# Optimization experiments

Measured on AMD Instinct MI355X. Metric: run time of the kernel, lower is better.

Reference implementation:

```python
import jax, jax.numpy as jnp
import numpy as np

EMBED_DIM = 2048
HIDDEN_DIM = 2048
SEQ_LEN = 8192


def setup_inputs() -> dict:
    key = jax.random.key(0)
    ks = jax.random.split(key, 6)
    x = jax.random.normal(ks[0], (SEQ_LEN, EMBED_DIM), dtype=jnp.float32)
    # original uses torch.rand (uniform [0,1)) for params
    W_h = jax.random.uniform(ks[1], (HIDDEN_DIM, HIDDEN_DIM), dtype=jnp.float32)
    W_x = jax.random.uniform(ks[2], (HIDDEN_DIM, EMBED_DIM), dtype=jnp.float32)
    W_y = jax.random.uniform(ks[3], (EMBED_DIM, HIDDEN_DIM), dtype=jnp.float32)
    B_h = jax.random.uniform(ks[4], (HIDDEN_DIM,), dtype=jnp.float32)
    B_y = jax.random.uniform(ks[5], (EMBED_DIM,), dtype=jnp.float32)
    return {"x": x, "W_h": W_h, "W_x": W_x, "W_y": W_y, "B_h": B_h, "B_y": B_y}


def reference(x, W_h, W_x, W_y, B_h, B_y):
    # Precompute input projections for all timesteps in one GEMM: [T, H]
    xp = x @ W_x.T + B_h

    def step(h, xp_t):
        h_new = jnp.tanh(W_h @ h + xp_t)  # [H]
        return h_new, h_new

    h0 = jnp.zeros((W_h.shape[0],), dtype=x.dtype)
    h_final, hs = jax.lax.scan(step, h0, xp)  # hs: [T, H]
    # Output projection + softmax over embed dim, batched over timesteps
    logits = hs @ W_y.T + B_y  # [T, E]
    output = jax.nn.softmax(logits, axis=-1)
    return (h_final, output)
```

## Files before the change

### kernel.cpp

```cpp
#include <hip/hip_runtime.h>

#define T_SEQ 8192
#define HDIM  2048
#define EDIM  2048
#define RBLK  64
#define ROWS_PER_BLK (HDIM / RBLK)

typedef unsigned long long u64;
typedef __attribute__((ext_vector_type(4))) unsigned int u32x4;
typedef __attribute__((ext_vector_type(4))) float f32x4;

__device__ inline void poll_pair(const u64* p0, const u64* p1, u32x4& a, u32x4& b) {
    asm volatile("global_load_dwordx4 %0, %2, off sc1\n\t"
                 "global_load_dwordx4 %1, %3, off sc1\n\t"
                 "s_waitcnt vmcnt(0)"
                 : "=v"(a), "=v"(b) : "v"(p0), "v"(p1) : "memory");
}

__device__ inline f32x4 ld_w16(const float* p) {
    f32x4 r;
    asm volatile("global_load_dwordx4 %0, %1, off" : "=v"(r) : "v"(p));
    return r;
}

__global__ __launch_bounds__(256) void gemm_nt_bias(
    const float* __restrict__ A, const float* __restrict__ B,
    const float* __restrict__ bias, float* __restrict__ C,
    int M, int N, int K)
{
    constexpr int BK = 32;
    __shared__ float As[BK][64 + 4];
    __shared__ float Bs[BK][64 + 4];

    const int tx = threadIdx.x & 15;
    const int ty = threadIdx.x >> 4;
    const int m0 = blockIdx.y * 64;
    const int n0 = blockIdx.x * 64;

    float acc[4][4] = {};

    for (int kk = 0; kk < K; kk += BK) {
        #pragma unroll
        for (int p = 0; p < 8; ++p) {
            int idx = p * 256 + threadIdx.x;
            int r = idx >> 5;
            int c = idx & 31;
            As[c][r] = A[(size_t)(m0 + r) * K + kk + c];
            Bs[c][r] = B[(size_t)(n0 + r) * K + kk + c];
        }
        __syncthreads();
        #pragma unroll
        for (int k = 0; k < BK; ++k) {
            float4 a = *(const float4*)&As[k][ty * 4];
            float4 b = *(const float4*)&Bs[k][tx * 4];
            float av[4] = {a.x, a.y, a.z, a.w};
            float bv[4] = {b.x, b.y, b.z, b.w};
            #pragma unroll
            for (int i = 0; i < 4; ++i)
                #pragma unroll
                for (int j = 0; j < 4; ++j)
                    acc[i][j] = fmaf(av[i], bv[j], acc[i][j]);
        }
        __syncthreads();
    }

    float4 bb = *(const float4*)&bias[n0 + tx * 4];
    float bvv[4] = {bb.x, bb.y, bb.z, bb.w};
    #pragma unroll
    for (int i = 0; i < 4; ++i) {
        float4 o;
        o.x = acc[i][0] + bvv[0];
        o.y = acc[i][1] + bvv[1];
        o.z = acc[i][2] + bvv[2];
        o.w = acc[i][3] + bvv[3];
        *(float4*)&C[(size_t)(m0 + ty * 4 + i) * N + n0 + tx * 4] = o;
    }
}

__global__ __launch_bounds__(512, 1) void rnn_recurrence(
    const float* __restrict__ Wh, const float* __restrict__ xp,
    float* __restrict__ Hs, u64* __restrict__ hbuf, int T)
{
    const int tid  = threadIdx.x;
    const int lane = tid & 63;
    const int wid  = tid >> 6;
    const int r0   = blockIdx.x * ROWS_PER_BLK + wid * 4;

    const float* wr0 = Wh + (size_t)(r0 + 0) * HDIM + lane * 4;
    const float* wr1 = Wh + (size_t)(r0 + 1) * HDIM + lane * 4;
    const float* wr2 = Wh + (size_t)(r0 + 2) * HDIM + lane * 4;
    const float* wr3 = Wh + (size_t)(r0 + 3) * HDIM + lane * 4;

    f32x4 w00 = ld_w16(wr0 + 0*256), w01 = ld_w16(wr0 + 1*256), w02 = ld_w16(wr0 + 2*256), w03 = ld_w16(wr0 + 3*256);
    f32x4 w04 = ld_w16(wr0 + 4*256), w05 = ld_w16(wr0 + 5*256), w06 = ld_w16(wr0 + 6*256), w07 = ld_w16(wr0 + 7*256);
    f32x4 w10 = ld_w16(wr1 + 0*256), w11 = ld_w16(wr1 + 1*256), w12 = ld_w16(wr1 + 2*256), w13 = ld_w16(wr1 + 3*256);
    f32x4 w14 = ld_w16(wr1 + 4*256), w15 = ld_w16(wr1 + 5*256), w16 = ld_w16(wr1 + 6*256), w17 = ld_w16(wr1 + 7*256);
    f32x4 w20 = ld_w16(wr2 + 0*256), w21 = ld_w16(wr2 + 1*256), w22 = ld_w16(wr2 + 2*256), w23 = ld_w16(wr2 + 3*256);
    f32x4 w24 = ld_w16(wr2 + 4*256), w25 = ld_w16(wr2 + 5*256), w26 = ld_w16(wr2 + 6*256), w27 = ld_w16(wr2 + 7*256);
    f32x4 w30 = ld_w16(wr3 + 0*256), w31 = ld_w16(wr3 + 1*256), w32 = ld_w16(wr3 + 2*256), w33 = ld_w16(wr3 + 3*256);
    f32x4 w34 = ld_w16(wr3 + 4*256), w35 = ld_w16(wr3 + 5*256), w36 = ld_w16(wr3 + 6*256), w37 = ld_w16(wr3 + 7*256);
    asm volatile("s_waitcnt vmcnt(0)" ::: "memory");

    __shared__ float hsm[HDIM];

    for (int t = 0; t < T; ++t) {
        float xq = 0.f;
        if (lane < 4) xq = xp[(size_t)t * HDIM + r0 + lane];

        float sv = 0.f;
        if (t > 0) {
            const u64* hb = hbuf + (size_t)(t & 1) * HDIM;
            const unsigned tg = (unsigned)t;
            const u64* p0 = hb + 2 * tid;
            const u64* p1 = hb + 1024 + 2 * tid;

            u32x4 a, b;
            poll_pair(p0, p1, a, b);
            while ((a.y != tg) | (a.w != tg) | (b.y != tg) | (b.w != tg))
                poll_pair(p0, p1, a, b);

            ((float2*)hsm)[tid] =
                make_float2(__uint_as_float(a.x), __uint_as_float(a.z));
            ((float2*)hsm)[tid + 512] =
                make_float2(__uint_as_float(b.x), __uint_as_float(b.z));
            __syncthreads();

            float s0 = 0.f, s1 = 0.f, s2 = 0.f, s3 = 0.f;
            #define RNN_STEP(IDX, WA, WB, WC, WD)                                   \
            {   float4 h4 = ((const float4*)hsm)[(IDX) * 64 + lane];                \
                s0 = fmaf(WA.x, h4.x, s0); s0 = fmaf(WA.y, h4.y, s0);               \
                s0 = fmaf(WA.z, h4.z, s0); s0 = fmaf(WA.w, h4.w, s0);               \
                s1 = fmaf(WB.x, h4.x, s1); s1 = fmaf(WB.y, h4.y, s1);               \
                s1 = fmaf(WB.z, h4.z, s1); s1 = fmaf(WB.w, h4.w, s1);               \
                s2 = fmaf(WC.x, h4.x, s2); s2 = fmaf(WC.y, h4.y, s2);               \
                s2 = fmaf(WC.z, h4.z, s2); s2 = fmaf(WC.w, h4.w, s2);               \
                s3 = fmaf(WD.x, h4.x, s3); s3 = fmaf(WD.y, h4.y, s3);               \
                s3 = fmaf(WD.z, h4.z, s3); s3 = fmaf(WD.w, h4.w, s3); }
            RNN_STEP(0, w00, w10, w20, w30)
            RNN_STEP(1, w01, w11, w21, w31)
            RNN_STEP(2, w02, w12, w22, w32)
            RNN_STEP(3, w03, w13, w23, w33)
            RNN_STEP(4, w04, w14, w24, w34)
            RNN_STEP(5, w05, w15, w25, w35)
            RNN_STEP(6, w06, w16, w26, w36)
            RNN_STEP(7, w07, w17, w27, w37)
            #undef RNN_STEP

            float fa = (lane & 1) ? s1 : s0;
            float fb = (lane & 1) ? s0 : s1;
            fa += __shfl_xor(fb, 1);
            float fc = (lane & 1) ? s3 : s2;
            float fd = (lane & 1) ? s2 : s3;
            fc += __shfl_xor(fd, 1);
            float fe = (lane & 2) ? fc : fa;
            float ff = (lane & 2) ? fa : fc;
            fe += __shfl_xor(ff, 2);
            #pragma unroll
            for (int off = 4; off < 64; off <<= 1) fe += __shfl_xor(fe, off);
            sv = fe;
        }

        if (lane < 4) {
            float hn = tanhf(sv + xq);
            u64 pk = ((u64)(unsigned)(t + 1) << 32) | (u64)__float_as_uint(hn);
            (void)__hip_atomic_exchange(
                &hbuf[(size_t)((t + 1) & 1) * HDIM + r0 + lane], pk,
                __ATOMIC_RELAXED, __HIP_MEMORY_SCOPE_AGENT);
            Hs[(size_t)t * HDIM + r0 + lane] = hn;
        }
    }
}

__global__ __launch_bounds__(256) void softmax_rows(
    const float* __restrict__ logits, float* __restrict__ out)
{
    const int row = blockIdx.x;
    const float4* in4 = (const float4*)(logits + (size_t)row * EDIM);
    float4* out4 = (float4*)(out + (size_t)row * EDIM);

    float4 v0 = in4[threadIdx.x];
    float4 v1 = in4[threadIdx.x + 256];

    float m = fmaxf(fmaxf(fmaxf(v0.x, v0.y), fmaxf(v0.z, v0.w)),
                    fmaxf(fmaxf(v1.x, v1.y), fmaxf(v1.z, v1.w)));
    #pragma unroll
    for (int off = 32; off > 0; off >>= 1) m = fmaxf(m, __shfl_xor(m, off));

    __shared__ float red[4];
    if ((threadIdx.x & 63) == 0) red[threadIdx.x >> 6] = m;
    __syncthreads();
    m = fmaxf(fmaxf(red[0], red[1]), fmaxf(red[2], red[3]));
    __syncthreads();

    float e[8];
    e[0] = expf(v0.x - m); e[1] = expf(v0.y - m);
    e[2] = expf(v0.z - m); e[3] = expf(v0.w - m);
    e[4] = expf(v1.x - m); e[5] = expf(v1.y - m);
    e[6] = expf(v1.z - m); e[7] = expf(v1.w - m);

    float s = e[0] + e[1] + e[2] + e[3] + e[4] + e[5] + e[6] + e[7];
    #pragma unroll
    for (int off = 32; off > 0; off >>= 1) s += __shfl_xor(s, off);
    if ((threadIdx.x & 63) == 0) red[threadIdx.x >> 6] = s;
    __syncthreads();
    s = red[0] + red[1] + red[2] + red[3];

    float inv = 1.0f / s;
    out4[threadIdx.x]       = make_float4(e[0] * inv, e[1] * inv, e[2] * inv, e[3] * inv);
    out4[threadIdx.x + 256] = make_float4(e[4] * inv, e[5] * inv, e[6] * inv, e[7] * inv);
}

__global__ void copy_vec(const float* __restrict__ src, float* __restrict__ dst, int n)
{
    int i = blockIdx.x * blockDim.x + threadIdx.x;
    if (i < n) dst[i] = src[i];
}

extern "C" void kernel_launch(void* const* d_in, const int* in_sizes, int n_in,
                              void* d_out, int out_size, void* d_ws, size_t ws_size,
                              hipStream_t stream)
{
    const float* x  = (const float*)d_in[0];
    const float* Wh = (const float*)d_in[1];
    const float* Wx = (const float*)d_in[2];
    const float* Wy = (const float*)d_in[3];
    const float* Bh = (const float*)d_in[4];
    const float* By = (const float*)d_in[5];

    float* out    = (float*)d_out;
    float* hfinal = out;
    float* hs     = out + HDIM;

    float* xp   = (float*)d_ws;
    u64*   hbuf = (u64*)((char*)d_ws + (size_t)T_SEQ * HDIM * 4);
    float* logits = xp;

    hipMemsetAsync(hbuf, 0, 2 * HDIM * sizeof(u64), stream);

    gemm_nt_bias<<<dim3(HDIM / 64, T_SEQ / 64), 256, 0, stream>>>(
        x, Wx, Bh, xp, T_SEQ, HDIM, EDIM);

    int T = T_SEQ;
    const float* xp_c = xp;
    void* args[] = {(void*)&Wh, (void*)&xp_c, (void*)&hs, (void*)&hbuf, (void*)&T};
    hipLaunchCooperativeKernel((void*)rnn_recurrence, dim3(RBLK), dim3(512),
                               args, 0, stream);

    gemm_nt_bias<<<dim3(EDIM / 64, T_SEQ / 64), 256, 0, stream>>>(
        hs, Wy, By, logits, T_SEQ, EDIM, HDIM);

    copy_vec<<<dim3(HDIM / 256), 256, 0, stream>>>(
        hs + (size_t)(T_SEQ - 1) * HDIM, hfinal, HDIM);

    softmax_rows<<<dim3(T_SEQ), 256, 0, stream>>>(logits, hs);
}
```

Before: 15.31 ms.

## Use split-bf16 MFMA GEMMs, transpose input projection, and fast tanh

```diff
diff --git a/kernel.cpp b/kernel.cpp
--- a/kernel.cpp
+++ b/kernel.cpp
@@ -9,6 +9,8 @@
 typedef unsigned long long u64;
 typedef __attribute__((ext_vector_type(4))) unsigned int u32x4;
 typedef __attribute__((ext_vector_type(4))) float f32x4;
+typedef __attribute__((ext_vector_type(8))) short bf16x8;
+typedef __attribute__((ext_vector_type(4))) short s16x4;
 
 __device__ inline void poll_pair(const u64* p0, const u64* p1, u32x4& a, u32x4& b) {
     asm volatile("global_load_dwordx4 %0, %2, off sc1\n\t"
@@ -23,62 +25,110 @@
     return r;
 }
 
-__global__ __launch_bounds__(256) void gemm_nt_bias(
+__device__ inline float fast_tanh(float z) {
+    float zc = fminf(fmaxf(z, -15.f), 15.f);
+    float zs = zc * 2.88539008177792681f;
+    float ez; asm("v_exp_f32 %0, %1" : "=v"(ez) : "v"(zs));
+    float rc; float ezp = ez + 1.f;
+    asm("v_rcp_f32 %0, %1" : "=v"(rc) : "v"(ezp));
+    return (ez - 1.f) * rc;
+}
+
+__device__ inline unsigned bf16_rne(float x) {
+    unsigned u = __float_as_uint(x);
+    return (u + 0x7fffu + ((u >> 16) & 1u)) >> 16;
+}
+__device__ inline void cvt_split4(float4 v, s16x4& h, s16x4& l) {
+    float xs[4] = {v.x, v.y, v.z, v.w};
+    #pragma unroll
+    for (int i = 0; i < 4; ++i) {
+        unsigned hb = bf16_rne(xs[i]);
+        float hf = __uint_as_float(hb << 16);
+        unsigned lb = bf16_rne(xs[i] - hf);
+        h[i] = (short)hb; l[i] = (short)lb;
+    }
+}
+
+__global__ __launch_bounds__(256) void gemm_mfma_split(
     const float* __restrict__ A, const float* __restrict__ B,
     const float* __restrict__ bias, float* __restrict__ C,
-    int M, int N, int K)
-{
-    constexpr int BK = 32;
-    __shared__ float As[BK][64 + 4];
-    __shared__ float Bs[BK][64 + 4];
-
-    const int tx = threadIdx.x & 15;
-    const int ty = threadIdx.x >> 4;
-    const int m0 = blockIdx.y * 64;
-    const int n0 = blockIdx.x * 64;
-
-    float acc[4][4] = {};
-
-    for (int kk = 0; kk < K; kk += BK) {
+    int M, int N, int K, int bias_per_row)
+{
+    __shared__ short Ah[128 * 32], Al[128 * 32];
+    __shared__ short Bh[128 * 32], Bl[128 * 32];
+
+    const int tid  = threadIdx.x;
+    const int lane = tid & 63;
+    const int wv   = tid >> 6;
+    const int wm   = (wv & 1) * 64;
+    const int wn   = (wv >> 1) * 64;
+    const int fr   = lane & 15;
+    const int fg   = lane >> 4;
+    const int m0   = blockIdx.y * 128;
+    const int n0   = blockIdx.x * 128;
+
+    f32x4 acc[4][4] = {};
+
+    for (int kk = 0; kk < K; kk += 32) {
         #pragma unroll
-        for (int p = 0; p < 8; ++p) {
-            int idx = p * 256 + threadIdx.x;
-            int r = idx >> 5;
-            int c = idx & 31;
-            As[c][r] = A[(size_t)(m0 + r) * K + kk + c];
-            Bs[c][r] = B[(size_t)(n0 + r) * K + kk + c];
+        for (int p = 0; p < 4; ++p) {
+            int idx = p * 256 + tid;
+            int r   = idx >> 3;
+            int c4  = idx & 7;
+            int boff = r * 64 + ((((c4 >> 1) ^ (r & 3)) << 4)) + (c4 & 1) * 8;
+            float4 va = *(const float4*)&A[(size_t)(m0 + r) * K + kk + c4 * 4];
+            float4 vb = *(const float4*)&B[(size_t)(n0 + r) * K + kk + c4 * 4];
+            s16x4 h, l;
+            cvt_split4(va, h, l);
+            *(s16x4*)((char*)Ah + boff) = h;
+            *(s16x4*)((char*)Al + boff) = l;
+            cvt_split4(vb, h, l);
+            *(s16x4*)((char*)Bh + boff) = h;
+            *(s16x4*)((char*)Bl + boff) = l;
         }
         __syncthreads();
+
+        const int ch = (fg ^ (fr & 3)) << 4;
+        bf16x8 ah[4], al[4], bh[4], bl[4];
         #pragma unroll
-        for (int k = 0; k < BK; ++k) {
-            float4 a = *(const float4*)&As[k][ty * 4];
-            float4 b = *(const float4*)&Bs[k][tx * 4];
-            float av[4] = {a.x, a.y, a.z, a.w};
-            float bv[4] = {b.x, b.y, b.z, b.w};
+        for (int i = 0; i < 4; ++i) {
+            int ar = (wm + i * 16 + fr) * 64 + ch;
+            int br = (wn + i * 16 + fr) * 64 + ch;
+            ah[i] = *(const bf16x8*)((const char*)Ah + ar);
+            al[i] = *(const bf16x8*)((const char*)Al + ar);
+            bh[i] = *(const bf16x8*)((const char*)Bh + br);
+            bl[i] = *(const bf16x8*)((const char*)Bl + br);
+        }
+
+        #pragma unroll
+        for (int i = 0; i < 4; ++i)
             #pragma unroll
-            for (int i = 0; i < 4; ++i)
-                #pragma unroll
-                for (int j = 0; j < 4; ++j)
-                    acc[i][j] = fmaf(av[i], bv[j], acc[i][j]);
-        }
+            for (int j = 0; j < 4; ++j) {
+                acc[i][j] = __builtin_amdgcn_mfma_f32_16x16x32_bf16(ah[i], bh[j], acc[i][j], 0, 0, 0);
+                acc[i][j] = __builtin_amdgcn_mfma_f32_16x16x32_bf16(ah[i], bl[j], acc[i][j], 0, 0, 0);
+                acc[i][j] = __builtin_amdgcn_mfma_f32_16x16x32_bf16(al[i], bh[j], acc[i][j], 0, 0, 0);
+            }
         __syncthreads();
     }
 
-    float4 bb = *(const float4*)&bias[n0 + tx * 4];
-    float bvv[4] = {bb.x, bb.y, bb.z, bb.w};
     #pragma unroll
     for (int i = 0; i < 4; ++i) {
-        float4 o;
-        o.x = acc[i][0] + bvv[0];
-        o.y = acc[i][1] + bvv[1];
-        o.z = acc[i][2] + bvv[2];
-        o.w = acc[i][3] + bvv[3];
-        *(float4*)&C[(size_t)(m0 + ty * 4 + i) * N + n0 + tx * 4] = o;
+        #pragma unroll
+        for (int r = 0; r < 4; ++r) {
+            int row = m0 + wm + i * 16 + fg * 4 + r;
+            float rb = bias_per_row ? bias[row] : 0.f;
+            #pragma unroll
+            for (int j = 0; j < 4; ++j) {
+                int col = n0 + wn + j * 16 + fr;
+                float bv = bias_per_row ? rb : bias[col];
+                C[(size_t)row * N + col] = acc[i][j][r] + bv;
+            }
+        }
     }
 }
 
 __global__ __launch_bounds__(512, 1) void rnn_recurrence(
-    const float* __restrict__ Wh, const float* __restrict__ xp,
+    const float* __restrict__ Wh, const float* __restrict__ xpT,
     float* __restrict__ Hs, u64* __restrict__ hbuf, int T)
 {
     const int tid  = threadIdx.x;
@@ -105,7 +155,7 @@
 
     for (int t = 0; t < T; ++t) {
         float xq = 0.f;
-        if (lane < 4) xq = xp[(size_t)t * HDIM + r0 + lane];
+        if (lane < 4) xq = xpT[(size_t)(r0 + lane) * T + t];
 
         float sv = 0.f;
         if (t > 0) {
@@ -161,7 +211,7 @@
         }
 
         if (lane < 4) {
-            float hn = tanhf(sv + xq);
+            float hn = fast_tanh(sv + xq);
             u64 pk = ((u64)(unsigned)(t + 1) << 32) | (u64)__float_as_uint(hn);
             (void)__hip_atomic_exchange(
                 &hbuf[(size_t)((t + 1) & 1) * HDIM + r0 + lane], pk,
@@ -231,23 +281,23 @@
     float* hfinal = out;
     float* hs     = out + HDIM;
 
-    float* xp   = (float*)d_ws;
+    float* xpT  = (float*)d_ws;
     u64*   hbuf = (u64*)((char*)d_ws + (size_t)T_SEQ * HDIM * 4);
-    float* logits = xp;
+    float* logits = xpT;
 
     hipMemsetAsync(hbuf, 0, 2 * HDIM * sizeof(u64), stream);
 
-    gemm_nt_bias<<<dim3(HDIM / 64, T_SEQ / 64), 256, 0, stream>>>(
-        x, Wx, Bh, xp, T_SEQ, HDIM, EDIM);
+    gemm_mfma_split<<<dim3(T_SEQ / 128, HDIM / 128), 256, 0, stream>>>(
+        Wx, x, Bh, xpT, HDIM, T_SEQ, EDIM, 1);
 
     int T = T_SEQ;
-    const float* xp_c = xp;
-    void* args[] = {(void*)&Wh, (void*)&xp_c, (void*)&hs, (void*)&hbuf, (void*)&T};
+    const float* xpT_c = xpT;
+    void* args[] = {(void*)&Wh, (void*)&xpT_c, (void*)&hs, (void*)&hbuf, (void*)&T};
     hipLaunchCooperativeKernel((void*)rnn_recurrence, dim3(RBLK), dim3(512),
                                args, 0, stream);
 
-    gemm_nt_bias<<<dim3(EDIM / 64, T_SEQ / 64), 256, 0, stream>>>(
-        hs, Wy, By, logits, T_SEQ, EDIM, HDIM);
+    gemm_mfma_split<<<dim3(EDIM / 128, T_SEQ / 128), 256, 0, stream>>>(
+        hs, Wy, By, logits, T_SEQ, EDIM, HDIM, 0);
 
     copy_vec<<<dim3(HDIM / 256), 256, 0, stream>>>(
         hs + (size_t)(T_SEQ - 1) * HDIM, hfinal, HDIM);
```

Result: faster. 13.24 ms (-13.5%).
